# Kernel optimization log

Measured on AMD Instinct MI355X. Metric: run time of the kernel, lower is better.

Reference implementation:

```python
import jax, jax.numpy as jnp
import numpy as np

D_MODEL = 768
N_HEADS = 12
D_FF = 3072
EPS = 1e-6


def setup_inputs() -> dict:
    key = jax.random.key(0)
    ks = jax.random.split(key, 9)
    s = 0.02
    return {
        "x": jax.random.normal(ks[0], (2, 4096, D_MODEL), dtype=jnp.float32),
        "wq": jax.random.normal(ks[1], (D_MODEL, D_MODEL), dtype=jnp.float32) * s,
        "wk": jax.random.normal(ks[2], (D_MODEL, D_MODEL), dtype=jnp.float32) * s,
        "wv": jax.random.normal(ks[3], (D_MODEL, D_MODEL), dtype=jnp.float32) * s,
        "wo": jax.random.normal(ks[4], (D_MODEL, D_MODEL), dtype=jnp.float32) * s,
        "w1": jax.random.normal(ks[5], (D_MODEL, D_FF), dtype=jnp.float32) * s,
        "b1": jnp.zeros((D_FF,), dtype=jnp.float32),
        "w2": jax.random.normal(ks[6], (D_FF, D_MODEL), dtype=jnp.float32) * s,
        "b2": jnp.zeros((D_MODEL,), dtype=jnp.float32),
        "g1": jnp.ones((D_MODEL,), dtype=jnp.float32),
        "g2": jnp.ones((D_MODEL,), dtype=jnp.float32),
    }


def _rmsnorm(x, g):
    rms = jax.lax.rsqrt(jnp.mean(x * x, axis=-1, keepdims=True) + EPS)
    return x * rms * g


def _attn(x, wq, wk, wv, wo):
    B, T, D = x.shape
    H, Dh = N_HEADS, D // N_HEADS
    q = (x @ wq).reshape(B, T, H, Dh).transpose(0, 2, 1, 3)
    k = (x @ wk).reshape(B, T, H, Dh).transpose(0, 2, 1, 3)
    v = (x @ wv).reshape(B, T, H, Dh).transpose(0, 2, 1, 3)
    scores = jnp.einsum("bhqd,bhkd->bhqk", q, k) * (Dh ** -0.5)
    causal = jnp.triu(jnp.ones((T, T), dtype=bool), k=1)
    scores = jnp.where(causal, -jnp.inf, scores)
    attn = jax.nn.softmax(scores, axis=-1)
    out = jnp.einsum("bhqk,bhkd->bhqd", attn, v)
    out = out.transpose(0, 2, 1, 3).reshape(B, T, D)
    return out @ wo


def _ffn(x, w1, b1, w2, b2):
    h = jax.nn.gelu(x @ w1 + b1, approximate=False)
    return h @ w2 + b2


def reference(x, wq, wk, wv, wo, w1, b1, w2, b2, g1, g2):
    x = x + _attn(_rmsnorm(x, g1), wq, wk, wv, wo)
    x = x + _ffn(_rmsnorm(x, g2), w1, b1, w2, b2)
    return x
```

## Files before the change

### kernel.cpp

```cpp
#include <hip/hip_runtime.h>
#include <hip/hip_bf16.h>

typedef __attribute__((ext_vector_type(8))) short bf16x8;
typedef __attribute__((ext_vector_type(4))) short bf16x4;
typedef __attribute__((ext_vector_type(4))) float f32x4;

#define MFMA16(a, b, c) __builtin_amdgcn_mfma_f32_16x16x32_bf16((a), (b), (c), 0, 0, 0)

__device__ __forceinline__ f32x4 mfma_k16(bf16x4 a, bf16x4 b, f32x4 c) {
#if __has_builtin(__builtin_amdgcn_mfma_f32_16x16x16bf16_1k)
  return __builtin_amdgcn_mfma_f32_16x16x16bf16_1k(a, b, c, 0, 0, 0);
#elif __has_builtin(__builtin_amdgcn_mfma_f32_16x16x16_bf16)
  return __builtin_amdgcn_mfma_f32_16x16x16_bf16(a, b, c, 0, 0, 0);
#else
  asm("v_mfma_f32_16x16x16_bf16 %0, %1, %2, %0" : "+v"(c) : "v"(a), "v"(b));
  return c;
#endif
}

__device__ __forceinline__ ushort f2bf(float f) {
  union { __hip_bfloat16 h; ushort u; } cv;
  cv.h = __float2bfloat16(f);
  return cv.u;
}

__device__ __forceinline__ float bf2f(ushort u) {
  union { float f; unsigned int i; } c;
  c.i = ((unsigned int)u) << 16;
  return c.f;
}

__device__ __forceinline__ void gload16(const void* g, void* l) {
  __builtin_amdgcn_global_load_lds((const __attribute__((address_space(1))) void*)g,
                                   (__attribute__((address_space(3))) void*)l, 16, 0, 0);
}

__global__ void wtrans_all(const float* __restrict__ wq, const float* __restrict__ wk,
                           const float* __restrict__ wv, const float* __restrict__ wo,
                           const float* __restrict__ w1, const float* __restrict__ w2,
                           ushort* __restrict__ wqT, ushort* __restrict__ wkT,
                           ushort* __restrict__ wvT, ushort* __restrict__ woT,
                           ushort* __restrict__ w1T, ushort* __restrict__ w2T) {
  __shared__ float t[32][33];
  int id = blockIdx.x;
  const float* W;
  ushort* Wt;
  int K, N, nbx;
  if (id < 2304) {
    const int m = id / 576;
    id -= m * 576;
    W = (m == 0) ? wq : (m == 1) ? wk : (m == 2) ? wv : wo;
    Wt = (m == 0) ? wqT : (m == 1) ? wkT : (m == 2) ? wvT : woT;
    K = 768; N = 768; nbx = 24;
  } else if (id < 4608) {
    id -= 2304; W = w1; Wt = w1T; K = 768; N = 3072; nbx = 96;
  } else {
    id -= 4608; W = w2; Wt = w2T; K = 3072; N = 768; nbx = 24;
  }
  const int nb = (id % nbx) * 32, kb = (id / nbx) * 32;
  const int tx = threadIdx.x & 31, ty = threadIdx.x >> 5;
#pragma unroll
  for (int i = 0; i < 4; ++i)
    t[ty + i * 8][tx] = W[(size_t)(kb + ty + i * 8) * N + nb + tx];
  __syncthreads();
#pragma unroll
  for (int i = 0; i < 4; ++i)
    Wt[(size_t)(nb + ty + i * 8) * K + kb + tx] = f2bf(t[tx][ty + i * 8]);
}

__global__ void rmsnorm_kernel(const float* __restrict__ x, const float* __restrict__ g,
                               ushort* __restrict__ out) {
  const int row = blockIdx.x, t = threadIdx.x;
  const float4 v = *(const float4*)(x + (size_t)row * 768 + 4 * t);
  float ss = v.x * v.x + v.y * v.y + v.z * v.z + v.w * v.w;
#pragma unroll
  for (int off = 1; off < 64; off <<= 1) ss += __shfl_xor(ss, off);
  __shared__ float part[3];
  if ((t & 63) == 0) part[t >> 6] = ss;
  __syncthreads();
  const float tot = part[0] + part[1] + part[2];
  const float r = rsqrtf(tot * (1.0f / 768.0f) + 1e-6f);
  const float4 gg = *(const float4*)(g + 4 * t);
  ushort4 o;
  o.x = f2bf(v.x * r * gg.x);
  o.y = f2bf(v.y * r * gg.y);
  o.z = f2bf(v.z * r * gg.z);
  o.w = f2bf(v.w * r * gg.w);
  *(ushort4*)(out + (size_t)row * 768 + 4 * t) = o;
}

enum { EPI_BF16 = 0, EPI_VT = 1, EPI_RESID = 2, EPI_BIAS_GELU = 3, EPI_BIAS_RESID = 4 };

template <int EPI>
__global__ __launch_bounds__(256) void gemm_bt(
    const ushort* __restrict__ A, const ushort* __restrict__ Bt, void* __restrict__ Cout,
    const float* __restrict__ bias, const float* __restrict__ resid, int M, int N, int K,
    float scale) {
  __shared__ ushort As[2][128 * 64];
  __shared__ ushort Bs[2][128 * 64];
  const int tid = threadIdx.x;
  const int lane = tid & 63, wid = tid >> 6;
  const int wm = wid >> 1, wn = wid & 1;
  const int l15 = lane & 15, l4 = lane >> 4;
  const int m0 = blockIdx.y * 128, n0 = blockIdx.x * 128;
  const int srow = lane >> 3, sslot = lane & 7;
  const int skel = (sslot ^ srow) << 3;

  f32x4 acc[4][4] = {};

#pragma unroll
  for (int i = 0; i < 4; ++i) {
    const int c = i * 4 + wid;
    const int row = c * 8 + srow;
    gload16(A + (size_t)(m0 + row) * K + skel, (char*)As[0] + c * 1024);
    gload16(Bt + (size_t)(n0 + row) * K + skel, (char*)Bs[0] + c * 1024);
  }

  int cur = 0;
  for (int k0 = 0; k0 < K; k0 += 64) {
    if (k0 + 64 < K) {
      char* dA = (char*)As[cur ^ 1];
      char* dB = (char*)Bs[cur ^ 1];
#pragma unroll
      for (int i = 0; i < 4; ++i) {
        const int c = i * 4 + wid;
        const int row = c * 8 + srow;
        gload16(A + (size_t)(m0 + row) * K + k0 + 64 + skel, dA + c * 1024);
        gload16(Bt + (size_t)(n0 + row) * K + k0 + 64 + skel, dB + c * 1024);
      }
      asm volatile("s_waitcnt vmcnt(8)" ::: "memory");
    } else {
      asm volatile("s_waitcnt vmcnt(0)" ::: "memory");
    }
    __builtin_amdgcn_s_barrier();

    const char* pA = (const char*)As[cur];
    const char* pB = (const char*)Bs[cur];
#pragma unroll
    for (int ks = 0; ks < 2; ++ks) {
      bf16x8 af[4], bfr[4];
#pragma unroll
      for (int mi = 0; mi < 4; ++mi) {
        const int row = wm * 64 + mi * 16 + l15;
        const int slot = (ks * 4 + l4) ^ (row & 7);
        af[mi] = *(const bf16x8*)(pA + row * 128 + slot * 16);
      }
#pragma unroll
      for (int ni = 0; ni < 4; ++ni) {
        const int row = wn * 64 + ni * 16 + l15;
        const int slot = (ks * 4 + l4) ^ (row & 7);
        bfr[ni] = *(const bf16x8*)(pB + row * 128 + slot * 16);
      }
#pragma unroll
      for (int mi = 0; mi < 4; ++mi)
#pragma unroll
        for (int ni = 0; ni < 4; ++ni)
          acc[mi][ni] = MFMA16(af[mi], bfr[ni], acc[mi][ni]);
    }
    asm volatile("" ::: "memory");
    __builtin_amdgcn_s_barrier();
    cur ^= 1;
  }

#pragma unroll
  for (int mi = 0; mi < 4; ++mi) {
#pragma unroll
    for (int ni = 0; ni < 4; ++ni) {
      const int gm = m0 + wm * 64 + mi * 16 + l4 * 4;
      const int gn = n0 + wn * 64 + ni * 16 + l15;
      f32x4 v = acc[mi][ni];
#pragma unroll
      for (int r = 0; r < 4; ++r) {
        const size_t idx = (size_t)(gm + r) * N + gn;
        const float f = v[r];
        if constexpr (EPI == EPI_BF16) {
          ((ushort*)Cout)[idx] = f2bf(f * scale);
        } else if constexpr (EPI == EPI_RESID) {
          ((float*)Cout)[idx] = f + resid[idx];
        } else if constexpr (EPI == EPI_BIAS_GELU) {
          const float u = f + bias[gn];
          const float gl = 0.5f * u * (1.0f + erff(u * 0.70710678118654752f));
          ((ushort*)Cout)[idx] = f2bf(gl);
        } else if constexpr (EPI == EPI_BIAS_RESID) {
          ((float*)Cout)[idx] = f + bias[gn] + resid[idx];
        }
      }
    }
  }
}

__global__ __launch_bounds__(256) void gemm_qkv(
    const ushort* __restrict__ A, const ushort* __restrict__ Bt,
    ushort* __restrict__ qout, ushort* __restrict__ kout, ushort* __restrict__ vtout,
    int M, int K, float qscale) {
  __shared__ ushort As[2][128 * 64];
  __shared__ ushort Bs[2][128 * 64];
  const int tid = threadIdx.x;
  const int lane = tid & 63, wid = tid >> 6;
  const int wm = wid >> 1, wn = wid & 1;
  const int l15 = lane & 15, l4 = lane >> 4;
  const int m0 = blockIdx.y * 128, n0 = blockIdx.x * 128;
  const int srow = lane >> 3, sslot = lane & 7;
  const int skel = (sslot ^ srow) << 3;

  f32x4 acc[4][4] = {};

#pragma unroll
  for (int i = 0; i < 4; ++i) {
    const int c = i * 4 + wid;
    const int row = c * 8 + srow;
    gload16(A + (size_t)(m0 + row) * K + skel, (char*)As[0] + c * 1024);
    gload16(Bt + (size_t)(n0 + row) * K + skel, (char*)Bs[0] + c * 1024);
  }

  int cur = 0;
  for (int k0 = 0; k0 < K; k0 += 64) {
    if (k0 + 64 < K) {
      char* dA = (char*)As[cur ^ 1];
      char* dB = (char*)Bs[cur ^ 1];
#pragma unroll
      for (int i = 0; i < 4; ++i) {
        const int c = i * 4 + wid;
        const int row = c * 8 + srow;
        gload16(A + (size_t)(m0 + row) * K + k0 + 64 + skel, dA + c * 1024);
        gload16(Bt + (size_t)(n0 + row) * K + k0 + 64 + skel, dB + c * 1024);
      }
      asm volatile("s_waitcnt vmcnt(8)" ::: "memory");
    } else {
      asm volatile("s_waitcnt vmcnt(0)" ::: "memory");
    }
    __builtin_amdgcn_s_barrier();

    const char* pA = (const char*)As[cur];
    const char* pB = (const char*)Bs[cur];
#pragma unroll
    for (int ks = 0; ks < 2; ++ks) {
      bf16x8 af[4], bfr[4];
#pragma unroll
      for (int mi = 0; mi < 4; ++mi) {
        const int row = wm * 64 + mi * 16 + l15;
        const int slot = (ks * 4 + l4) ^ (row & 7);
        af[mi] = *(const bf16x8*)(pA + row * 128 + slot * 16);
      }
#pragma unroll
      for (int ni = 0; ni < 4; ++ni) {
        const int row = wn * 64 + ni * 16 + l15;
        const int slot = (ks * 4 + l4) ^ (row & 7);
        bfr[ni] = *(const bf16x8*)(pB + row * 128 + slot * 16);
      }
#pragma unroll
      for (int mi = 0; mi < 4; ++mi)
#pragma unroll
        for (int ni = 0; ni < 4; ++ni)
          acc[mi][ni] = MFMA16(af[mi], bfr[ni], acc[mi][ni]);
    }
    asm volatile("" ::: "memory");
    __builtin_amdgcn_s_barrier();
    cur ^= 1;
  }

  const int seg = n0 / 768;
#pragma unroll
  for (int mi = 0; mi < 4; ++mi) {
#pragma unroll
    for (int ni = 0; ni < 4; ++ni) {
      const int gm = m0 + wm * 64 + mi * 16 + l4 * 4;
      const int gn = n0 + wn * 64 + ni * 16 + l15;
      const int col = gn - seg * 768;
      f32x4 v = acc[mi][ni];
      if (seg == 0) {
#pragma unroll
        for (int r = 0; r < 4; ++r)
          qout[(size_t)(gm + r) * 768 + col] = f2bf(v[r] * qscale);
      } else if (seg == 1) {
#pragma unroll
        for (int r = 0; r < 4; ++r)
          kout[(size_t)(gm + r) * 768 + col] = f2bf(v[r]);
      } else {
        const int b = gm >> 12, tt = gm & 4095;
        const int h = col >> 6, dh = col & 63;
        ushort4 pk;
        pk.x = f2bf(v[0]); pk.y = f2bf(v[1]); pk.z = f2bf(v[2]); pk.w = f2bf(v[3]);
        *(ushort4*)(vtout + (((size_t)(b * 12 + h) * 64 + dh) * 4096 + tt)) = pk;
      }
    }
  }
}

__global__ __launch_bounds__(256, 5) void flash_attn_kernel(
    const ushort* __restrict__ Q, const ushort* __restrict__ Kb,
    const ushort* __restrict__ Vt, ushort* __restrict__ Opart,
    float* __restrict__ dsb) {
  __shared__ ushort Ks[2][64 * 64];
  __shared__ ushort Vts[2][64 * 64];
  const int tid = threadIdx.x, lane = tid & 63, wid = tid >> 6;
  const int l15 = lane & 15, l4 = lane >> 4;
  const int l7 = l15 & 7;
  const int bid = (int)blockIdx.x;
  const int idx = (bid & 7) * 384 + (bid >> 3);
  const int pair = idx >> 1, half = idx & 1;
  const int bh = pair >> 6, b = bh / 12, h = bh % 12;
  const int qb = 63 - (pair & 63);
  const int qbase = qb * 64;
  const int q0 = qbase + wid * 16;
  const int nt = qb + 1;
  const int h0 = nt >> 1;
  const int kt0 = half ? h0 : 0;
  const int kt1 = half ? nt : h0;

  bf16x8 qf0, qf1;
  {
    const ushort* qp = Q + ((size_t)(b * 4096 + q0 + l15) * 768 + h * 64 + l4 * 8);
    qf0 = *(const bf16x8*)qp;
    qf1 = *(const bf16x8*)(qp + 32);
  }
  f32x4 oo[4] = {};
  float dsum = 0.f;

  const int srow_l = lane >> 3;
  const int sco = ((lane & 7) ^ srow_l) << 3;
  const ushort* Kbase = Kb + (size_t)b * 4096 * 768 + h * 64;
  const ushort* Vbase = Vt + (size_t)bh * 64 * 4096;
  const int c0 = wid, c1 = 4 + wid;
  const ushort* kp0 = Kbase + (size_t)(kt0 * 64 + c0 * 8 + srow_l) * 768 + sco;
  const ushort* kp1 = Kbase + (size_t)(kt0 * 64 + c1 * 8 + srow_l) * 768 + sco;
  const ushort* vp0 = Vbase + (size_t)(c0 * 8 + srow_l) * 4096 + kt0 * 64 + sco;
  const ushort* vp1 = Vbase + (size_t)(c1 * 8 + srow_l) * 4096 + kt0 * 64 + sco;

  const int koff0 = l15 * 128 + ((l4 ^ l7) << 4);
  const int koff1 = l15 * 128 + (((4 + l4) ^ l7) << 4);
  const int vbase_off = l15 * 128 + ((l4 & 1) << 3);
  const int t2b = l4 >> 1;

  if (kt0 < kt1) {
    gload16(kp0, (char*)Ks + c0 * 1024);
    gload16(kp1, (char*)Ks + c1 * 1024);
    gload16(vp0, (char*)Vts + c0 * 1024);
    gload16(vp1, (char*)Vts + c1 * 1024);
  }

  int cur = 0;
  for (int kt = kt0; kt < kt1; ++kt) {
    const int k0 = kt << 6;
    if (kt + 1 < kt1) {
      kp0 += 64 * 768; kp1 += 64 * 768;
      vp0 += 64; vp1 += 64;
      const int nb = (cur ^ 1) * 8192;
      gload16(kp0, (char*)Ks + nb + c0 * 1024);
      gload16(kp1, (char*)Ks + nb + c1 * 1024);
      gload16(vp0, (char*)Vts + nb + c0 * 1024);
      gload16(vp1, (char*)Vts + nb + c1 * 1024);
      asm volatile("s_waitcnt vmcnt(4)" ::: "memory");
    } else {
      asm volatile("s_waitcnt vmcnt(0)" ::: "memory");
    }
    __builtin_amdgcn_s_barrier();

    const int nf = (q0 + 16 - k0) >> 4;
    const int nct = nf < 4 ? nf : 4;
    const bool has_diag = (nf <= 4);
    const char* Kc = (const char*)Ks + cur * 8192;
    const char* Vc = (const char*)Vts + cur * 8192;

    __builtin_amdgcn_s_setprio(1);
#pragma unroll
    for (int ct = 0; ct < 4; ++ct) {
      if (ct < nct) {
        f32x4 s = {0.f, 0.f, 0.f, 0.f};
        const bf16x8 kf0 = *(const bf16x8*)(Kc + ct * 2048 + koff0);
        const bf16x8 kf1 = *(const bf16x8*)(Kc + ct * 2048 + koff1);
        s = MFMA16(kf0, qf0, s);
        s = MFMA16(kf1, qf1, s);
        if (has_diag && ct == nct - 1) {
#pragma unroll
          for (int r = 0; r < 4; ++r)
            if (l4 * 4 + r > l15) s[r] = -30.f;
        }
        const float p0 = __builtin_amdgcn_exp2f(s[0]);
        const float p1 = __builtin_amdgcn_exp2f(s[1]);
        const float p2 = __builtin_amdgcn_exp2f(s[2]);
        const float p3 = __builtin_amdgcn_exp2f(s[3]);
        dsum += (p0 + p1) + (p2 + p3);
        union { bf16x4 v; ushort u[4]; } pk;
        pk.u[0] = f2bf(p0); pk.u[1] = f2bf(p1);
        pk.u[2] = f2bf(p2); pk.u[3] = f2bf(p3);
        const int xo = ((2 * ct + t2b) ^ l7) << 4;
#pragma unroll
        for (int dt = 0; dt < 4; ++dt) {
          const bf16x4 vf = *(const bf16x4*)(Vc + dt * 2048 + vbase_off + xo);
          oo[dt] = mfma_k16(pk.v, vf, oo[dt]);
        }
      }
    }
    __builtin_amdgcn_s_setprio(0);
    asm volatile("" ::: "memory");
    __builtin_amdgcn_s_barrier();
    cur ^= 1;
  }

  dsum += __shfl_xor(dsum, 16);
  dsum += __shfl_xor(dsum, 32);
  if (l4 == 0)
    dsb[((half * 24 + b * 12 + h) << 12) + q0 + l15] = dsum;
  ushort* op = Opart + ((size_t)(half * 8192 + b * 4096 + q0 + l4 * 4)) * 768 + h * 64;
#pragma unroll
  for (int r = 0; r < 4; ++r) {
#pragma unroll
    for (int dt = 0; dt < 4; ++dt)
      op[(size_t)r * 768 + dt * 16 + l15] = f2bf(oo[dt][r]);
  }
}

__global__ void attn_merge(const ushort* __restrict__ P, const float* __restrict__ ds,
                           ushort* __restrict__ attn) {
  const int row = blockIdx.x, t = threadIdx.x;
  const int b = row >> 12, tr = row & 4095;
  __shared__ float inv[12];
  if (t < 12) {
    const float d0 = ds[((b * 12 + t) << 12) + tr];
    const float d1 = ds[((24 + b * 12 + t) << 12) + tr];
    inv[t] = 1.0f / (d0 + d1);
  }
  __syncthreads();
  const size_t o0 = (size_t)row * 768 + 4 * t;
  const ushort4 a = *(const ushort4*)(P + o0);
  const ushort4 c = *(const ushort4*)(P + (size_t)8192 * 768 + o0);
  const float iv = inv[t >> 4];
  ushort4 o;
  o.x = f2bf((bf2f(a.x) + bf2f(c.x)) * iv);
  o.y = f2bf((bf2f(a.y) + bf2f(c.y)) * iv);
  o.z = f2bf((bf2f(a.z) + bf2f(c.z)) * iv);
  o.w = f2bf((bf2f(a.w) + bf2f(c.w)) * iv);
  *(ushort4*)(attn + o0) = o;
}

extern "C" void kernel_launch(void* const* d_in, const int* in_sizes, int n_in,
                              void* d_out, int out_size, void* d_ws, size_t ws_size,
                              hipStream_t stream) {
  const float* x  = (const float*)d_in[0];
  const float* wq = (const float*)d_in[1];
  const float* wk = (const float*)d_in[2];
  const float* wv = (const float*)d_in[3];
  const float* wo = (const float*)d_in[4];
  const float* w1 = (const float*)d_in[5];
  const float* b1 = (const float*)d_in[6];
  const float* w2 = (const float*)d_in[7];
  const float* b2 = (const float*)d_in[8];
  const float* g1 = (const float*)d_in[9];
  const float* g2 = (const float*)d_in[10];
  float* out = (float*)d_out;

  char* p = (char*)d_ws;
  ushort* wqT = (ushort*)p; p += (size_t)768 * 768 * 2;
  ushort* wkT = (ushort*)p; p += (size_t)768 * 768 * 2;
  ushort* wvT = (ushort*)p; p += (size_t)768 * 768 * 2;
  ushort* woT = (ushort*)p; p += (size_t)768 * 768 * 2;
  ushort* w1T = (ushort*)p; p += (size_t)3072 * 768 * 2;
  ushort* w2T = (ushort*)p; p += (size_t)768 * 3072 * 2;
  ushort* xn  = (ushort*)p; p += (size_t)8192 * 768 * 2;
  ushort* qb  = (ushort*)p; p += (size_t)8192 * 768 * 2;
  ushort* kb  = (ushort*)p; p += (size_t)8192 * 768 * 2;
  ushort* vtb = (ushort*)p; p += (size_t)8192 * 768 * 2;
  ushort* attn = (ushort*)p; p += (size_t)8192 * 768 * 2;
  float* x2 = (float*)p; p += (size_t)8192 * 768 * 4;
  float* dsb = (float*)p; p += (size_t)2 * 24 * 4096 * 4;
  ushort* hf = qb;
  ushort* Opart = (ushort*)x2;

  const float qscale = 0.125f * 1.44269504088896340736f;

  dim3 blk(256);
  wtrans_all<<<dim3(6912), blk, 0, stream>>>(wq, wk, wv, wo, w1, w2,
                                             wqT, wkT, wvT, woT, w1T, w2T);

  rmsnorm_kernel<<<8192, dim3(192), 0, stream>>>(x, g1, xn);

  gemm_qkv<<<dim3(18, 64), blk, 0, stream>>>(xn, wqT, qb, kb, vtb, 8192, 768, qscale);

  flash_attn_kernel<<<dim3(3072), blk, 0, stream>>>(qb, kb, vtb, Opart, dsb);

  attn_merge<<<dim3(8192), dim3(192), 0, stream>>>(Opart, dsb, attn);

  gemm_bt<EPI_RESID><<<dim3(6, 64), blk, 0, stream>>>(attn, woT, x2, nullptr, x, 8192, 768, 768, 1.0f);

  rmsnorm_kernel<<<8192, dim3(192), 0, stream>>>(x2, g2, xn);

  gemm_bt<EPI_BIAS_GELU><<<dim3(24, 64), blk, 0, stream>>>(xn, w1T, hf, b1, nullptr, 8192, 3072, 768, 1.0f);
  gemm_bt<EPI_BIAS_RESID><<<dim3(6, 64), blk, 0, stream>>>(hf, w2T, out, b2, x2, 8192, 768, 3072, 1.0f);
}
```

Before: 328.4 us.

## Use 256x256-tile eight-wave pipelined GEMM for QKV and FFN1 projections

Adds a 256x256-tile GEMM core with 512 threads. Each wave holds a 128x64 accumulator, and the k-loop is split into phases that overlap half-tile global-to-LDS loads with MFMA work. It uses staged vmcnt waits and s_setprio around the MFMA bursts. The QKV projection and the first FFN GEMM with bias+GELU move to this kernel, aiming for more data reuse per LDS byte and better latency hiding. The cost is 128KB of LDS per block, which limits occupancy to one block per CU, and coarse grids (288 and 384 blocks) that may leave a partial last wave.

Result: slower. 359.0 us (+9.3%).

```diff
diff --git a/kernel.cpp b/kernel.cpp
--- a/kernel.cpp
+++ b/kernel.cpp
@@ -189,82 +189,143 @@
   }
 }
 
-__global__ __launch_bounds__(256) void gemm_qkv(
+#define G256_VM8 asm volatile("s_waitcnt vmcnt(8)" ::: "memory")
+#define G256_VM4 asm volatile("s_waitcnt vmcnt(4)" ::: "memory")
+#define G256_VM0 asm volatile("s_waitcnt vmcnt(0)" ::: "memory")
+#define G256_NOP (void)0
+
+#define G256_PHASE(BUF, KH, MH, STAGE, TAILW)                                  \
+  {                                                                            \
+    asm volatile("" ::: "memory");                                             \
+    const char* Ab_ = AsB + (BUF) * 32768 + (KH) * 16384 + aro;                \
+    const char* Bb_ = BsB + (BUF) * 32768 + (KH) * 16384 + bro;                \
+    bf16x8 af_[4], bf_[4];                                                     \
+    _Pragma("unroll") for (int i_ = 0; i_ < 4; ++i_)                           \
+        af_[i_] = *(const bf16x8*)(Ab_ + (MH) * 4096 + i_ * 1024);             \
+    _Pragma("unroll") for (int i_ = 0; i_ < 4; ++i_)                           \
+        bf_[i_] = *(const bf16x8*)(Bb_ + i_ * 1024);                           \
+    STAGE;                                                                     \
+    __builtin_amdgcn_s_barrier();                                              \
+    __builtin_amdgcn_s_setprio(1);                                             \
+    _Pragma("unroll") for (int i_ = 0; i_ < 4; ++i_)                           \
+        _Pragma("unroll") for (int n_ = 0; n_ < 4; ++n_)                       \
+            acc[(MH) * 4 + i_][n_] =                                           \
+                MFMA16(af_[i_], bf_[n_], acc[(MH) * 4 + i_][n_]);              \
+    __builtin_amdgcn_s_setprio(0);                                             \
+    TAILW;                                                                     \
+    asm volatile("" ::: "memory");                                             \
+    __builtin_amdgcn_s_barrier();                                              \
+  }
+
+__device__ __forceinline__ void gemm256_core(const ushort* __restrict__ A,
+                                             const ushort* __restrict__ Bt, int K,
+                                             int m0, int n0, char* AsB, char* BsB,
+                                             f32x4 (&acc)[8][4]) {
+  const int tid = threadIdx.x, lane = tid & 63, wid = tid >> 6;
+  const int l15 = lane & 15, l4 = lane >> 4;
+  const int wm = wid >> 2, wn = wid & 3;
+  const int aro = (wm * 128 + l15) * 64 + l4 * 16;
+  const int bro = (wn * 64 + l15) * 64 + l4 * 16;
+
+  const ushort* pA0 = A + (size_t)(m0 + (tid >> 2)) * K + ((tid & 3) << 3);
+  const ushort* pB0 = Bt + (size_t)(n0 + (tid >> 2)) * K + ((tid & 3) << 3);
+  const int wofs = wid << 10;
+
+  auto stA = [&](int kt, int kh, int buf) {
+    const ushort* s = pA0 + kt * 64 + kh * 32;
+    char* d = AsB + buf * 32768 + kh * 16384 + wofs;
+    gload16(s, d);
+    gload16(s + (size_t)128 * K, d + 8192);
+  };
+  auto stB = [&](int kt, int kh, int buf) {
+    const ushort* s = pB0 + kt * 64 + kh * 32;
+    char* d = BsB + buf * 32768 + kh * 16384 + wofs;
+    gload16(s, d);
+    gload16(s + (size_t)128 * K, d + 8192);
+  };
+
+  stA(0, 0, 0); stB(0, 0, 0);
+  stA(0, 1, 0); stB(0, 1, 0);
+  stA(1, 0, 1); stB(1, 0, 1);
+  G256_VM8;
+  __builtin_amdgcn_s_barrier();
+
+  const int niter = K >> 7;
+  for (int j = 0; j < niter - 1; ++j) {
+    const int t1 = 2 * j + 1, t2 = 2 * j + 2, t3 = 2 * j + 3;
+    G256_PHASE(0, 0, 0, stA(t1, 1, 1), G256_NOP)
+    G256_PHASE(0, 0, 1, stB(t1, 1, 1), G256_VM8)
+    G256_PHASE(0, 1, 0, stA(t2, 0, 0), G256_NOP)
+    G256_PHASE(0, 1, 1, stB(t2, 0, 0), G256_VM8)
+    G256_PHASE(1, 0, 0, stA(t2, 1, 0), G256_NOP)
+    G256_PHASE(1, 0, 1, stB(t2, 1, 0), G256_VM8)
+    G256_PHASE(1, 1, 0, stA(t3, 0, 1), G256_NOP)
+    G256_PHASE(1, 1, 1, stB(t3, 0, 1), G256_VM8)
+  }
+  {
+    const int t1 = (K >> 6) - 1;
+    G256_PHASE(0, 0, 0, stA(t1, 1, 1), G256_NOP)
+    G256_PHASE(0, 0, 1, stB(t1, 1, 1), G256_VM8)
+    G256_PHASE(0, 1, 0, G256_NOP, G256_NOP)
+    G256_PHASE(0, 1, 1, G256_NOP, G256_VM4)
+    G256_PHASE(1, 0, 0, G256_NOP, G256_NOP)
+    G256_PHASE(1, 0, 1, G256_NOP, G256_VM0)
+    G256_PHASE(1, 1, 0, G256_NOP, G256_NOP)
+    G256_PHASE(1, 1, 1, G256_NOP, G256_NOP)
+  }
+}
+
+__global__ __launch_bounds__(512, 2) void gemm256_gelu(
+    const ushort* __restrict__ A, const ushort* __restrict__ Bt,
+    ushort* __restrict__ Cout, const float* __restrict__ bias, int N, int K) {
+  __shared__ char AsB[65536];
+  __shared__ char BsB[65536];
+  const int tid = threadIdx.x, lane = tid & 63, wid = tid >> 6;
+  const int l15 = lane & 15, l4 = lane >> 4;
+  const int wm = wid >> 2, wn = wid & 3;
+  const int m0 = blockIdx.y * 256, n0 = blockIdx.x * 256;
+
+  f32x4 acc[8][4] = {};
+  gemm256_core(A, Bt, K, m0, n0, AsB, BsB, acc);
+
+#pragma unroll
+  for (int mi = 0; mi < 8; ++mi) {
+#pragma unroll
+    for (int ni = 0; ni < 4; ++ni) {
+      const int gm = m0 + wm * 128 + mi * 16 + l4 * 4;
+      const int gn = n0 + wn * 64 + ni * 16 + l15;
+      const float bv = bias[gn];
+      f32x4 v = acc[mi][ni];
+#pragma unroll
+      for (int r = 0; r < 4; ++r) {
+        const float u = v[r] + bv;
+        const float gl = 0.5f * u * (1.0f + erff(u * 0.70710678118654752f));
+        Cout[(size_t)(gm + r) * N + gn] = f2bf(gl);
+      }
+    }
+  }
+}
+
+__global__ __launch_bounds__(512, 2) void gemm256_qkv(
     const ushort* __restrict__ A, const ushort* __restrict__ Bt,
     ushort* __restrict__ qout, ushort* __restrict__ kout, ushort* __restrict__ vtout,
-    int M, int K, float qscale) {
-  __shared__ ushort As[2][128 * 64];
-  __shared__ ushort Bs[2][128 * 64];
-  const int tid = threadIdx.x;
-  const int lane = tid & 63, wid = tid >> 6;
-  const int wm = wid >> 1, wn = wid & 1;
+    int K, float qscale) {
+  __shared__ char AsB[65536];
+  __shared__ char BsB[65536];
+  const int tid = threadIdx.x, lane = tid & 63, wid = tid >> 6;
   const int l15 = lane & 15, l4 = lane >> 4;
-  const int m0 = blockIdx.y * 128, n0 = blockIdx.x * 128;
-  const int srow = lane >> 3, sslot = lane & 7;
-  const int skel = (sslot ^ srow) << 3;
-
-  f32x4 acc[4][4] = {};
-
-#pragma unroll
-  for (int i = 0; i < 4; ++i) {
-    const int c = i * 4 + wid;
-    const int row = c * 8 + srow;
-    gload16(A + (size_t)(m0 + row) * K + skel, (char*)As[0] + c * 1024);
-    gload16(Bt + (size_t)(n0 + row) * K + skel, (char*)Bs[0] + c * 1024);
-  }
-
-  int cur = 0;
-  for (int k0 = 0; k0 < K; k0 += 64) {
-    if (k0 + 64 < K) {
-      char* dA = (char*)As[cur ^ 1];
-      char* dB = (char*)Bs[cur ^ 1];
-#pragma unroll
-      for (int i = 0; i < 4; ++i) {
-        const int c = i * 4 + wid;
-        const int row = c * 8 + srow;
-        gload16(A + (size_t)(m0 + row) * K + k0 + 64 + skel, dA + c * 1024);
-        gload16(Bt + (size_t)(n0 + row) * K + k0 + 64 + skel, dB + c * 1024);
-      }
-      asm volatile("s_waitcnt vmcnt(8)" ::: "memory");
-    } else {
-      asm volatile("s_waitcnt vmcnt(0)" ::: "memory");
-    }
-    __builtin_amdgcn_s_barrier();
-
-    const char* pA = (const char*)As[cur];
-    const char* pB = (const char*)Bs[cur];
-#pragma unroll
-    for (int ks = 0; ks < 2; ++ks) {
-      bf16x8 af[4], bfr[4];
-#pragma unroll
-      for (int mi = 0; mi < 4; ++mi) {
-        const int row = wm * 64 + mi * 16 + l15;
-        const int slot = (ks * 4 + l4) ^ (row & 7);
-        af[mi] = *(const bf16x8*)(pA + row * 128 + slot * 16);
-      }
-#pragma unroll
-      for (int ni = 0; ni < 4; ++ni) {
-        const int row = wn * 64 + ni * 16 + l15;
-        const int slot = (ks * 4 + l4) ^ (row & 7);
-        bfr[ni] = *(const bf16x8*)(pB + row * 128 + slot * 16);
-      }
-#pragma unroll
-      for (int mi = 0; mi < 4; ++mi)
-#pragma unroll
-        for (int ni = 0; ni < 4; ++ni)
-          acc[mi][ni] = MFMA16(af[mi], bfr[ni], acc[mi][ni]);
-    }
-    asm volatile("" ::: "memory");
-    __builtin_amdgcn_s_barrier();
-    cur ^= 1;
-  }
+  const int wm = wid >> 2, wn = wid & 3;
+  const int m0 = blockIdx.y * 256, n0 = blockIdx.x * 256;
+
+  f32x4 acc[8][4] = {};
+  gemm256_core(A, Bt, K, m0, n0, AsB, BsB, acc);
 
   const int seg = n0 / 768;
 #pragma unroll
-  for (int mi = 0; mi < 4; ++mi) {
+  for (int mi = 0; mi < 8; ++mi) {
 #pragma unroll
     for (int ni = 0; ni < 4; ++ni) {
-      const int gm = m0 + wm * 64 + mi * 16 + l4 * 4;
+      const int gm = m0 + wm * 128 + mi * 16 + l4 * 4;
       const int gn = n0 + wn * 64 + ni * 16 + l15;
       const int col = gn - seg * 768;
       f32x4 v = acc[mi][ni];
@@ -475,7 +536,7 @@
 
   rmsnorm_kernel<<<8192, dim3(192), 0, stream>>>(x, g1, xn);
 
-  gemm_qkv<<<dim3(18, 64), blk, 0, stream>>>(xn, wqT, qb, kb, vtb, 8192, 768, qscale);
+  gemm256_qkv<<<dim3(9, 32), dim3(512), 0, stream>>>(xn, wqT, qb, kb, vtb, 768, qscale);
 
   flash_attn_kernel<<<dim3(3072), blk, 0, stream>>>(qb, kb, vtb, Opart, dsb);
 
@@ -485,6 +546,7 @@
 
   rmsnorm_kernel<<<8192, dim3(192), 0, stream>>>(x2, g2, xn);
 
-  gemm_bt<EPI_BIAS_GELU><<<dim3(24, 64), blk, 0, stream>>>(xn, w1T, hf, b1, nullptr, 8192, 3072, 768, 1.0f);
+  gemm256_gelu<<<dim3(12, 32), dim3(512), 0, stream>>>(xn, w1T, hf, b1, 3072, 768);
+
   gemm_bt<EPI_BIAS_RESID><<<dim3(6, 64), blk, 0, stream>>>(hf, w2T, out, b2, x2, 8192, 768, 3072, 1.0f);
 }
```
